# Kernel optimization log

Measured on AMD Instinct MI355X. Metric: run time of the kernel, lower is better.

The kernel has to match this reference:

```python
import math
import jax, jax.numpy as jnp
import numpy as np

B, S, D, H = 4, 1024, 768, 12  # batch, seq, hidden, heads (ViT-Base)
HD = D // H                     # head size = 64
EPS = 1e-12                     # F.normalize eps


def setup_inputs() -> dict:
    key = jax.random.key(0)
    ks = jax.random.split(key, 7)
    s = 0.02
    return {
        "hidden_states": jax.random.normal(ks[0], (B, S, D), dtype=jnp.float32),
        "Wq": jax.random.normal(ks[1], (D, D), dtype=jnp.float32) * s,
        "bq": jax.random.normal(ks[2], (D,), dtype=jnp.float32) * s,
        "Wv": jax.random.normal(ks[3], (D, D), dtype=jnp.float32) * s,
        "bv": jax.random.normal(ks[4], (D,), dtype=jnp.float32) * s,
        "Wo": jax.random.normal(ks[5], (D, D), dtype=jnp.float32) * s,
        "bo": jax.random.normal(ks[6], (D,), dtype=jnp.float32) * s,
    }


def _split_heads(x):
    # [B,S,D] -> [B,H,S,hd]
    b, s, _ = x.shape
    return x.reshape(b, s, H, HD).transpose(0, 2, 1, 3)


def reference(hidden_states, Wq, bq, Wv, bv, Wo, bo):
    b, s, d_model = hidden_states.shape
    # Linear layers (torch Linear: x @ W^T + b; here W stored already transposed)
    mixed_q = hidden_states @ Wq + bq          # key == query in this module
    mixed_v = hidden_states @ Wv + bv
    q = _split_heads(mixed_q)                  # [B,H,S,hd]
    v = _split_heads(mixed_v)                  # [B,H,S,hd]

    # symmetric self-attention (Q @ Q^T)
    scores = jnp.einsum("bhsd,bhtd->bhst", q, q) / math.sqrt(HD)
    probs1 = jax.nn.softmax(scores, axis=-1)                 # [B,H,S,S]
    probs = 0.5 * (probs1 + probs1.transpose(0, 1, 3, 2))    # symmetrize

    # F.normalize(value_layer, dim=2): L2-normalize along the SEQUENCE axis
    vnorm = jnp.maximum(jnp.sqrt(jnp.sum(v * v, axis=2, keepdims=True)), EPS)
    V = v / vnorm                                            # [B,H,S,hd]

    # random-walk Laplacian: D^{-1}(D - P) = I - P / rowsum  (diag structure exploited,
    # same math as diag_embed + matmul in the original)
    dvec = probs.sum(axis=3)                                 # [B,H,S]
    Pn = probs / dvec[..., :, None]                          # D^{-1} P
    LrwV = V - jnp.einsum("bhst,bhtd->bhsd", Pn, V)          # L_rw @ V

    # trace( sum_{b,h} V^T L_rw V ) = sum over all (b,h,s,d) of V * (L_rw V)
    denom = jnp.float32(HD * H * b)
    tr = jnp.abs(jnp.sum(V * LrwV)) / denom

    # orthogonality regularizer: sum (V^T V - I)^2
    VtV = jnp.einsum("bhsd,bhse->bhde", V, V)                # [B,H,hd,hd]
    regular_term = jnp.sum((VtV - jnp.eye(HD, dtype=V.dtype)) ** 2) / denom

    # context = P @ V  (is_last=False)
    ctx = jnp.einsum("bhst,bhtd->bhsd", probs, v)
    ctx = ctx.transpose(0, 2, 1, 3).reshape(b, s, d_model)
    attention_output = ctx @ Wo + bo                         # dropout = identity (p=0)
    return (attention_output, tr, regular_term, mixed_q, mixed_q)
```

## Files before the change

### kernel.cpp

```cpp
#include <hip/hip_runtime.h>
#include <math.h>

constexpr float SCALE = 0.125f;

typedef __attribute__((ext_vector_type(8))) short bf8;
typedef __attribute__((ext_vector_type(8))) unsigned short u16x8;
typedef __attribute__((ext_vector_type(4))) float f32x4;

static __device__ __forceinline__ unsigned short f2bf(float f) {
    unsigned int u = __float_as_uint(f);
    u += 0x7fffu + ((u >> 16) & 1u);
    return (unsigned short)(u >> 16);
}
static __device__ __forceinline__ float bf2f(unsigned short h) {
    return __uint_as_float(((unsigned int)h) << 16);
}
static __device__ __forceinline__ bf8 ld8(const unsigned short* p) {
    return *reinterpret_cast<const bf8*>(p);
}
static __device__ __forceinline__ unsigned int cvtpk(float lo, float hi) {
    unsigned int r;
    asm("v_cvt_pk_bf16_f32 %0, %1, %2" : "=v"(r) : "v"(lo), "v"(hi));
    return r;
}

__global__ __launch_bounds__(256)
void k_prep(const float* __restrict__ Wq, const float* __restrict__ Wv,
            unsigned short* __restrict__ WTq, unsigned short* __restrict__ WTv)
{
    __shared__ unsigned short T[64 * 72];
    const int bid = blockIdx.x;
    const bool isQ = (bid < 144);
    const int lb = isQ ? bid : bid - 144;
    const float* __restrict__ W = isQ ? Wq : Wv;
    unsigned short* __restrict__ WT = isQ ? WTq : WTv;
    const int n0 = (lb % 12) * 64;
    const int k0 = (lb / 12) * 64;
    const int tid = threadIdx.x;
    const int r  = tid >> 2;
    const int c0 = (tid & 3) * 16;
    const float* src = &W[(size_t)(k0 + r) * 768 + n0 + c0];
    #pragma unroll
    for (int q = 0; q < 4; ++q) {
        const float4 v = *reinterpret_cast<const float4*>(src + q * 4);
        uint2 pk;
        pk.x = cvtpk(v.x, v.y);
        pk.y = cvtpk(v.z, v.w);
        *reinterpret_cast<uint2*>(&T[r * 72 + c0 + q * 4]) = pk;
    }
    __syncthreads();
    const int n  = tid >> 2;
    const int kc = (tid & 3) * 16;
    u16x8 o0, o1;
    #pragma unroll
    for (int i = 0; i < 8; ++i) o0[i] = T[(kc + i) * 72 + n];
    #pragma unroll
    for (int i = 0; i < 8; ++i) o1[i] = T[(kc + 8 + i) * 72 + n];
    unsigned short* dst = WT + (size_t)(n0 + n) * 768 + k0 + kc;
    *reinterpret_cast<u16x8*>(dst)     = o0;
    *reinterpret_cast<u16x8*>(dst + 8) = o1;
}

__global__ __launch_bounds__(256)
void k_gemm_qv(const float* __restrict__ X,
               const unsigned short* __restrict__ WTq,
               const unsigned short* __restrict__ WTv,
               const float* __restrict__ bq, const float* __restrict__ bv,
               float* __restrict__ mq1, float* __restrict__ mq2,
               unsigned short* __restrict__ qb, unsigned short* __restrict__ mvb)
{
    __shared__ unsigned short As[64 * 72];
    __shared__ unsigned short Bs[128 * 72];
    const int m0 = blockIdx.x * 64;
    const bool isQ = (blockIdx.y < 6);
    const int n0 = (isQ ? blockIdx.y : blockIdx.y - 6) * 128;
    const unsigned short* __restrict__ WT = isQ ? WTq : WTv;
    const float* __restrict__ bias = isQ ? bq : bv;
    const int tid = threadIdx.x;
    const int wave = tid >> 6, lane = tid & 63, lm = lane & 15, lg = lane >> 4;
    const int wn = wave;

    f32x4 acc[4][2];
    #pragma unroll
    for (int mi = 0; mi < 4; ++mi)
        #pragma unroll
        for (int ni = 0; ni < 2; ++ni) acc[mi][ni] = (f32x4){0.f, 0.f, 0.f, 0.f};

    for (int k0 = 0; k0 < 768; k0 += 64) {
        #pragma unroll
        for (int it = 0; it < 4; ++it) {
            const int idx = tid + it * 256;
            const int arow = idx >> 4;
            const int ac4  = (idx & 15) * 4;
            const float4 v = *reinterpret_cast<const float4*>(
                &X[(size_t)(m0 + arow) * 768 + k0 + ac4]);
            uint2 pk;
            pk.x = cvtpk(v.x, v.y);
            pk.y = cvtpk(v.z, v.w);
            *reinterpret_cast<uint2*>(&As[arow * 72 + ac4]) = pk;
            const int brow = idx >> 3;
            const int bc8  = (idx & 7) * 8;
            *reinterpret_cast<u16x8*>(&Bs[brow * 72 + bc8]) =
                *reinterpret_cast<const u16x8*>(&WT[(size_t)(n0 + brow) * 768 + k0 + bc8]);
        }
        __syncthreads();
        #pragma unroll
        for (int ks = 0; ks < 2; ++ks) {
            bf8 af[4], bfr[2];
            #pragma unroll
            for (int mi = 0; mi < 4; ++mi)
                af[mi] = *reinterpret_cast<const bf8*>(
                    &As[(mi * 16 + lm) * 72 + ks * 32 + lg * 8]);
            #pragma unroll
            for (int ni = 0; ni < 2; ++ni)
                bfr[ni] = *reinterpret_cast<const bf8*>(
                    &Bs[(wn * 32 + ni * 16 + lm) * 72 + ks * 32 + lg * 8]);
            #pragma unroll
            for (int mi = 0; mi < 4; ++mi)
                #pragma unroll
                for (int ni = 0; ni < 2; ++ni)
                    acc[mi][ni] = __builtin_amdgcn_mfma_f32_16x16x32_bf16(
                        af[mi], bfr[ni], acc[mi][ni], 0, 0, 0);
        }
        __syncthreads();
    }
    #pragma unroll
    for (int ni = 0; ni < 2; ++ni) {
        const int c = n0 + wn * 32 + ni * 16 + lm;
        const float bcol = bias[c];
        #pragma unroll
        for (int mi = 0; mi < 4; ++mi)
            #pragma unroll
            for (int j = 0; j < 4; ++j) {
                const int r = m0 + mi * 16 + lg * 4 + j;
                const float v = acc[mi][ni][j] + bcol;
                const size_t off = (size_t)r * 768 + c;
                if (isQ) {
                    mq1[off] = v;
                    mq2[off] = v;
                    qb[off]  = f2bf(v);
                } else {
                    mvb[off] = f2bf(v);
                }
            }
    }
}

__global__ __launch_bounds__(256)
void k_gemm_one(const unsigned short* __restrict__ Xb,
                const unsigned short* __restrict__ WT,
                const float* __restrict__ bias, float* __restrict__ out)
{
    __shared__ unsigned short As[64 * 72];
    __shared__ unsigned short Bs[64 * 72];
    const int m0 = blockIdx.x * 64;
    const int n0 = blockIdx.y * 64;
    const int tid = threadIdx.x;
    const int w = tid >> 6, lane = tid & 63, lm = lane & 15, lg = lane >> 4;

    f32x4 acc[4];
    #pragma unroll
    for (int ni = 0; ni < 4; ++ni) acc[ni] = (f32x4){0.f, 0.f, 0.f, 0.f};

    for (int k0 = 0; k0 < 768; k0 += 64) {
        #pragma unroll
        for (int it = 0; it < 2; ++it) {
            const int idx = tid + it * 256;
            const int row = idx >> 3;
            const int c8  = (idx & 7) * 8;
            *reinterpret_cast<u16x8*>(&As[row * 72 + c8]) =
                *reinterpret_cast<const u16x8*>(&Xb[(size_t)(m0 + row) * 768 + k0 + c8]);
            *reinterpret_cast<u16x8*>(&Bs[row * 72 + c8]) =
                *reinterpret_cast<const u16x8*>(&WT[(size_t)(n0 + row) * 768 + k0 + c8]);
        }
        __syncthreads();
        #pragma unroll
        for (int ks = 0; ks < 2; ++ks) {
            const bf8 af = *reinterpret_cast<const bf8*>(
                &As[(w * 16 + lm) * 72 + ks * 32 + lg * 8]);
            #pragma unroll
            for (int ni = 0; ni < 4; ++ni) {
                const bf8 bfr = *reinterpret_cast<const bf8*>(
                    &Bs[(ni * 16 + lm) * 72 + ks * 32 + lg * 8]);
                acc[ni] = __builtin_amdgcn_mfma_f32_16x16x32_bf16(af, bfr, acc[ni], 0, 0, 0);
            }
        }
        __syncthreads();
    }
    #pragma unroll
    for (int ni = 0; ni < 4; ++ni) {
        const int c = n0 + ni * 16 + lm;
        const float bcol = bias[c];
        #pragma unroll
        for (int j = 0; j < 4; ++j) {
            const int r = m0 + w * 16 + lg * 4 + j;
            out[(size_t)r * 768 + c] = acc[ni][j] + bcol;
        }
    }
}

__global__ __launch_bounds__(256)
void k_pass1T(const unsigned short* __restrict__ qb,
              const unsigned short* __restrict__ mvb,
              unsigned short* __restrict__ vT,
              float* __restrict__ a, float* __restrict__ nrmp)
{
    __shared__ __align__(16) unsigned short Kb[2][64 * 72];
    const int bid = blockIdx.x;
    const int st = (bid >> 3) & 15;
    const int bh = (bid & 7) + 8 * (bid >> 7);
    const int b = bh / 12, h = bh % 12;
    const int s0 = st * 64;
    const int tid = threadIdx.x;
    const int w = tid >> 6, lane = tid & 63, lm = lane & 15, lg = lane >> 4;
    const size_t qoff = (size_t)(b * 1024) * 768 + h * 64;

    {
        const int r  = tid >> 2;
        const int c0 = (tid & 3) * 16;
        const unsigned short* src = mvb + (size_t)(b * 1024 + s0 + r) * 768 + h * 64 + c0;
        const u16x8 x0 = *reinterpret_cast<const u16x8*>(src);
        const u16x8 x1 = *reinterpret_cast<const u16x8*>(src + 8);
        *reinterpret_cast<u16x8*>(&Kb[0][r * 72 + c0])     = x0;
        *reinterpret_cast<u16x8*>(&Kb[0][r * 72 + c0 + 8]) = x1;
        __syncthreads();
        const int dd  = tid >> 2;
        const int sc0 = (tid & 3) * 16;
        u16x8 o0, o1;
        float ps = 0.f;
        #pragma unroll
        for (int k = 0; k < 8; ++k) {
            o0[k] = Kb[0][(sc0 + k) * 72 + dd];
            const float v = bf2f(o0[k]);
            ps = fmaf(v, v, ps);
        }
        #pragma unroll
        for (int k = 0; k < 8; ++k) {
            o1[k] = Kb[0][(sc0 + 8 + k) * 72 + dd];
            const float v = bf2f(o1[k]);
            ps = fmaf(v, v, ps);
        }
        ps += __shfl_xor(ps, 1);
        ps += __shfl_xor(ps, 2);
        if ((tid & 3) == 0) nrmp[(size_t)(bh * 16 + st) * 64 + dd] = ps;
        unsigned short* dst = vT + (size_t)bh * 65536 + (size_t)dd * 1024 + s0 + sc0;
        *reinterpret_cast<u16x8*>(dst)     = o0;
        *reinterpret_cast<u16x8*>(dst + 8) = o1;
        __syncthreads();
    }

    const unsigned short* srow_p = qb + qoff + (size_t)(s0 + 16 * w + lm) * 768;
    const bf8 qs0 = ld8(srow_p + 8 * lg);
    const bf8 qs1 = ld8(srow_p + 32 + 8 * lg);
    const f32x4 z = {0.f, 0.f, 0.f, 0.f};
    float r = 0.f;
    const int sr = tid >> 2;
    const int sc = (tid & 3) << 4;

    u16x8 kr0 = *reinterpret_cast<const u16x8*>(qb + qoff + (size_t)sr * 768 + sc);
    u16x8 kr1 = *reinterpret_cast<const u16x8*>(qb + qoff + (size_t)sr * 768 + sc + 8);
    *reinterpret_cast<u16x8*>(&Kb[0][sr * 72 + sc])     = kr0;
    *reinterpret_cast<u16x8*>(&Kb[0][sr * 72 + sc + 8]) = kr1;
    __syncthreads();
    int cur = 0;

    for (int tt = 0; tt < 16; ++tt) {
        if (tt < 15) {
            const size_t rg = qoff + (size_t)((tt + 1) * 64 + sr) * 768 + sc;
            kr0 = *reinterpret_cast<const u16x8*>(qb + rg);
            kr1 = *reinterpret_cast<const u16x8*>(qb + rg + 8);
        }
        #pragma unroll
        for (int nf = 0; nf < 4; ++nf) {
            const bf8 ka0 = *reinterpret_cast<const bf8*>(
                &Kb[cur][(16 * nf + lm) * 72 + 8 * lg]);
            const bf8 ka1 = *reinterpret_cast<const bf8*>(
                &Kb[cur][(16 * nf + lm) * 72 + 32 + 8 * lg]);
            f32x4 ef = __builtin_amdgcn_mfma_f32_16x16x32_bf16(ka0, qs0, z, 0, 0, 0);
            ef = __builtin_amdgcn_mfma_f32_16x16x32_bf16(ka1, qs1, ef, 0, 0, 0);
            r += __expf(ef[0] * SCALE) + __expf(ef[1] * SCALE)
               + __expf(ef[2] * SCALE) + __expf(ef[3] * SCALE);
        }
        if (tt < 15) {
            *reinterpret_cast<u16x8*>(&Kb[cur ^ 1][sr * 72 + sc])     = kr0;
            *reinterpret_cast<u16x8*>(&Kb[cur ^ 1][sr * 72 + sc + 8]) = kr1;
        }
        __syncthreads();
        cur ^= 1;
    }
    r += __shfl_xor(r, 16);
    r += __shfl_xor(r, 32);
    if (lg == 0) a[(size_t)bh * 1024 + s0 + 16 * w + lm] = 1.f / r;
}

__global__ __launch_bounds__(256)
void k_normfin(const float* __restrict__ nrmp, float* __restrict__ inv_n,
               float* __restrict__ t1p)
{
    const int bh = blockIdx.x;
    const int tid = threadIdx.x;
    __shared__ float t1s[64];
    if (tid < 64) {
        float s = 0.f;
        for (int st = 0; st < 16; ++st)
            s += nrmp[(size_t)(bh * 16 + st) * 64 + tid];
        const float n = fmaxf(sqrtf(s), 1e-12f);
        const float iv = 1.f / n;
        inv_n[bh * 64 + tid] = iv;
        t1s[tid] = s * iv * iv;
    }
    __syncthreads();
    if (tid == 0) {
        float t = 0.f;
        for (int k = 0; k < 64; ++k) t += t1s[k];
        t1p[bh] = t;
    }
}

__global__ __launch_bounds__(256)
void k_pass2(const unsigned short* __restrict__ qb,
             const unsigned short* __restrict__ vT,
             const unsigned short* __restrict__ mvb,
             const float* __restrict__ a,
             const float* __restrict__ invn,
             unsigned short* __restrict__ ctxb,
             float* __restrict__ t2p)
{
    __shared__ __align__(16) unsigned short Kb[2][64 * 72];
    __shared__ __align__(16) unsigned short Vb[2][64 * 72];
    __shared__ __align__(16) unsigned short F_lds[4 * 16 * 72];
    __shared__ float red[256];
    const int bid = blockIdx.x;
    const int st = (bid >> 3) & 15;
    const int bh = (bid & 7) + 8 * (bid >> 7);
    const int b = bh / 12, h = bh % 12;
    const int s0 = st * 64;
    const int tid = threadIdx.x;
    const int w = tid >> 6, lane = tid & 63, lm = lane & 15, lg = lane >> 4;
    const size_t qoff = (size_t)(b * 1024) * 768 + h * 64;
    const unsigned short* srow_p = qb + qoff + (size_t)(s0 + 16 * w + lm) * 768;
    const bf8 qs0 = ld8(srow_p + 8 * lg);
    const bf8 qs1 = ld8(srow_p + 32 + 8 * lg);
    const unsigned short* vbase = vT + (size_t)bh * 65536;
    const float* abase = a + (size_t)bh * 1024;
    const float a_s = abase[s0 + 16 * w + lm];
    unsigned short* Frow = &F_lds[w * 1152 + lm * 72];
    float inv2[4];
    #pragma unroll
    for (int nf = 0; nf < 4; ++nf) {
        const float iv = invn[bh * 64 + lm + 16 * nf];
        inv2[nf] = iv * iv;
    }
    const f32x4 z = {0.f, 0.f, 0.f, 0.f};
    f32x4 acc[4];
    #pragma unroll
    for (int nf = 0; nf < 4; ++nf) acc[nf] = z;
    float sF = 0.f;
    const int sr = tid >> 2;
    const int sc = (tid & 3) << 4;

    u16x8 kr0 = *reinterpret_cast<const u16x8*>(qb + qoff + (size_t)sr * 768 + sc);
    u16x8 kr1 = *reinterpret_cast<const u16x8*>(qb + qoff + (size_t)sr * 768 + sc + 8);
    u16x8 vr0 = *reinterpret_cast<const u16x8*>(vbase + (size_t)sr * 1024 + sc);
    u16x8 vr1 = *reinterpret_cast<const u16x8*>(vbase + (size_t)sr * 1024 + sc + 8);
    *reinterpret_cast<u16x8*>(&Kb[0][sr * 72 + sc])     = kr0;
    *reinterpret_cast<u16x8*>(&Kb[0][sr * 72 + sc + 8]) = kr1;
    *reinterpret_cast<u16x8*>(&Vb[0][sr * 72 + sc])     = vr0;
    *reinterpret_cast<u16x8*>(&Vb[0][sr * 72 + sc + 8]) = vr1;
    __syncthreads();
    int cur = 0;

    for (int tt = 0; tt < 16; ++tt) {
        const int t0 = tt * 64;
        if (tt < 15) {
            const size_t kg = qoff + (size_t)(t0 + 64 + sr) * 768 + sc;
            kr0 = *reinterpret_cast<const u16x8*>(qb + kg);
            kr1 = *reinterpret_cast<const u16x8*>(qb + kg + 8);
            const size_t vg = (size_t)sr * 1024 + t0 + 64 + sc;
            vr0 = *reinterpret_cast<const u16x8*>(vbase + vg);
            vr1 = *reinterpret_cast<const u16x8*>(vbase + vg + 8);
        }
        f32x4 ef[4];
        #pragma unroll
        for (int nf = 0; nf < 4; ++nf) {
            const bf8 ka0 = *reinterpret_cast<const bf8*>(
                &Kb[cur][(16 * nf + lm) * 72 + 8 * lg]);
            const bf8 ka1 = *reinterpret_cast<const bf8*>(
                &Kb[cur][(16 * nf + lm) * 72 + 32 + 8 * lg]);
            ef[nf] = __builtin_amdgcn_mfma_f32_16x16x32_bf16(ka0, qs0, z, 0, 0, 0);
            ef[nf] = __builtin_amdgcn_mfma_f32_16x16x32_bf16(ka1, qs1, ef[nf], 0, 0, 0);
        }
        #pragma unroll
        for (int nf = 0; nf < 4; ++nf) {
            const float4 af = *reinterpret_cast<const float4*>(
                abase + t0 + 16 * nf + 4 * lg);
            const float f0 = __expf(ef[nf][0] * SCALE) * (a_s + af.x);
            const float f1 = __expf(ef[nf][1] * SCALE) * (a_s + af.y);
            const float f2 = __expf(ef[nf][2] * SCALE) * (a_s + af.z);
            const float f3 = __expf(ef[nf][3] * SCALE) * (a_s + af.w);
            sF += (f0 + f1) + (f2 + f3);
            uint2 pk;
            pk.x = cvtpk(f0, f1);
            pk.y = cvtpk(f2, f3);
            *reinterpret_cast<uint2*>(&Frow[16 * nf + 4 * lg]) = pk;
        }
        #pragma unroll
        for (int ks = 0; ks < 2; ++ks) {
            const bf8 fa = *reinterpret_cast<const bf8*>(&Frow[32 * ks + 8 * lg]);
            #pragma unroll
            for (int nf = 0; nf < 4; ++nf) {
                const bf8 vfr = *reinterpret_cast<const bf8*>(
                    &Vb[cur][(16 * nf + lm) * 72 + 32 * ks + 8 * lg]);
                acc[nf] = __builtin_amdgcn_mfma_f32_16x16x32_bf16(fa, vfr, acc[nf], 0, 0, 0);
            }
        }
        if (tt < 15) {
            *reinterpret_cast<u16x8*>(&Kb[cur ^ 1][sr * 72 + sc])     = kr0;
            *reinterpret_cast<u16x8*>(&Kb[cur ^ 1][sr * 72 + sc + 8]) = kr1;
            *reinterpret_cast<u16x8*>(&Vb[cur ^ 1][sr * 72 + sc])     = vr0;
            *reinterpret_cast<u16x8*>(&Vb[cur ^ 1][sr * 72 + sc + 8]) = vr1;
        }
        __syncthreads();
        cur ^= 1;
    }
    sF += __shfl_xor(sF, 16);
    sF += __shfl_xor(sF, 32);

    float t2 = 0.f;
    #pragma unroll
    for (int j = 0; j < 4; ++j) {
        const int srow = s0 + 16 * w + 4 * lg + j;
        const float sFj = __shfl(sF, 4 * lg + j);
        const float rdv = 2.f / sFj;
        const size_t rowoff = (size_t)(b * 1024 + srow) * 768 + h * 64;
        #pragma unroll
        for (int nf = 0; nf < 4; ++nf) {
            const int d = lm + 16 * nf;
            const float cf = 0.5f * acc[nf][j];
            ctxb[rowoff + d] = f2bf(cf);
            const float vv = bf2f(mvb[rowoff + d]);
            t2 = fmaf(vv * cf, inv2[nf] * rdv, t2);
        }
    }
    red[tid] = t2;
    __syncthreads();
    for (int k = 128; k >= 1; k >>= 1) {
        if (tid < k) red[tid] += red[tid + k];
        __syncthreads();
    }
    if (tid == 0) t2p[bh * 16 + st] = red[0];
}

__global__ __launch_bounds__(256)
void k_regwt(const unsigned short* __restrict__ vT, float* __restrict__ Gpart,
             const float* __restrict__ Wo, unsigned short* __restrict__ WTo)
{
    __shared__ unsigned short T[64 * 72];
    const int bid = blockIdx.x;
    const int tid = threadIdx.x;
    if (bid < 384) {
        const int bh = bid >> 3;
        const int q  = bid & 7;
        const int w = tid >> 6, lane = tid & 63, lm = lane & 15, lg = lane >> 4;
        const unsigned short* base = vT + (size_t)bh * 65536;
        const unsigned short* arowp = base + (size_t)(16 * w + lm) * 1024;
        const f32x4 z = {0.f, 0.f, 0.f, 0.f};
        f32x4 acc[4];
        #pragma unroll
        for (int nf = 0; nf < 4; ++nf) acc[nf] = z;
        #pragma unroll
        for (int kk = 0; kk < 4; ++kk) {
            const int t0 = (q * 4 + kk) * 32 + 8 * lg;
            const bf8 av = ld8(arowp + t0);
            #pragma unroll
            for (int nf = 0; nf < 4; ++nf) {
                const bf8 bv = ld8(base + (size_t)(lm + 16 * nf) * 1024 + t0);
                acc[nf] = __builtin_amdgcn_mfma_f32_16x16x32_bf16(av, bv, acc[nf], 0, 0, 0);
            }
        }
        float* gdst = Gpart + (size_t)(bh * 8 + q) * 4096;
        #pragma unroll
        for (int nf = 0; nf < 4; ++nf) {
            const int d2 = lm + 16 * nf;
            #pragma unroll
            for (int j = 0; j < 4; ++j) {
                const int d1 = 16 * w + 4 * lg + j;
                gdst[d1 * 64 + d2] = acc[nf][j];
            }
        }
    } else {
        const int lb = bid - 384;
        const int n0 = (lb % 12) * 64;
        const int k0 = (lb / 12) * 64;
        const int r  = tid >> 2;
        const int c0 = (tid & 3) * 16;
        const float* src = &Wo[(size_t)(k0 + r) * 768 + n0 + c0];
        #pragma unroll
        for (int q = 0; q < 4; ++q) {
            const float4 v = *reinterpret_cast<const float4*>(src + q * 4);
            uint2 pk;
            pk.x = cvtpk(v.x, v.y);
            pk.y = cvtpk(v.z, v.w);
            *reinterpret_cast<uint2*>(&T[r * 72 + c0 + q * 4]) = pk;
        }
        __syncthreads();
        const int n  = tid >> 2;
        const int kc = (tid & 3) * 16;
        u16x8 o0, o1;
        #pragma unroll
        for (int i = 0; i < 8; ++i) o0[i] = T[(kc + i) * 72 + n];
        #pragma unroll
        for (int i = 0; i < 8; ++i) o1[i] = T[(kc + 8 + i) * 72 + n];
        unsigned short* dst = WTo + (size_t)(n0 + n) * 768 + k0 + kc;
        *reinterpret_cast<u16x8*>(dst)     = o0;
        *reinterpret_cast<u16x8*>(dst + 8) = o1;
    }
}

__global__ __launch_bounds__(256)
void k_regfin(const float* __restrict__ Gpart, const float* __restrict__ invn,
              float* __restrict__ regp)
{
    const int bh = blockIdx.x;
    const int tid = threadIdx.x;
    float part = 0.f;
    for (int c = tid; c < 4096; c += 256) {
        const int d1 = c >> 6, d2 = c & 63;
        float g = 0.f;
        #pragma unroll
        for (int q = 0; q < 8; ++q)
            g += Gpart[(size_t)(bh * 8 + q) * 4096 + c];
        g *= invn[bh * 64 + d1] * invn[bh * 64 + d2];
        const float diff = g - ((d1 == d2) ? 1.f : 0.f);
        part = fmaf(diff, diff, part);
    }
    __shared__ float red[256];
    red[tid] = part;
    __syncthreads();
    for (int k = 128; k >= 1; k >>= 1) {
        if (tid < k) red[tid] += red[tid + k];
        __syncthreads();
    }
    if (tid == 0) regp[bh] = red[0];
}

__global__ __launch_bounds__(256)
void k_final(const float* __restrict__ t1p, const float* __restrict__ t2p,
             const float* __restrict__ regp, float* __restrict__ out_tr,
             float* __restrict__ out_reg)
{
    const int tid = threadIdx.x;
    float s1 = 0.f, s2 = 0.f, s3 = 0.f;
    for (int i = tid; i < 768; i += 256) s2 += t2p[i];
    if (tid < 48) { s1 = t1p[tid]; s3 = regp[tid]; }
    __shared__ float R1[256];
    __shared__ float R2[256];
    __shared__ float R3[256];
    R1[tid] = s1; R2[tid] = s2; R3[tid] = s3;
    __syncthreads();
    for (int w = 128; w >= 1; w >>= 1) {
        if (tid < w) { R1[tid] += R1[tid + w]; R2[tid] += R2[tid + w]; R3[tid] += R3[tid + w]; }
        __syncthreads();
    }
    if (tid == 0) {
        *out_tr  = fabsf(R1[0] - R2[0]) / 3072.f;
        *out_reg = R3[0] / 3072.f;
    }
}

extern "C" void kernel_launch(void* const* d_in, const int* in_sizes, int n_in,
                              void* d_out, int out_size, void* d_ws, size_t ws_size,
                              hipStream_t stream)
{
    const float* X  = (const float*)d_in[0];
    const float* Wq = (const float*)d_in[1];
    const float* bq = (const float*)d_in[2];
    const float* Wv = (const float*)d_in[3];
    const float* bv = (const float*)d_in[4];
    const float* Wo = (const float*)d_in[5];
    const float* bo = (const float*)d_in[6];

    float* out = (float*)d_out;
    float* att = out;
    float* tr  = out + 3145728;
    float* rg  = out + 3145729;
    float* mq1 = out + 3145730;
    float* mq2 = out + 6291458;

    float* ws = (float*)d_ws;
    unsigned short* mvb  = (unsigned short*)(ws);
    unsigned short* WTo  = (unsigned short*)(ws);
    unsigned short* qb   = (unsigned short*)(ws + 1572864);
    float*          Gpart = ws + 1572864;
    unsigned short* vTslot = (unsigned short*)(ws + 3145728);
    unsigned short* WTq  = vTslot;
    unsigned short* WTv  = vTslot + 589824;
    unsigned short* vT   = vTslot;
    unsigned short* ctxb = (unsigned short*)(ws + 4718592);
    float* nrmp = ws + 6291456;
    float* aarr = ws + 6389760;
    float* invn = ws + 6438960;
    float* t1p  = ws + 6442032;
    float* t2p  = ws + 6442080;
    float* regp = ws + 6442848;

    if (ws_size < (size_t)6442896 * sizeof(float)) return;

    k_prep     <<<288,          256, 0, stream>>>(Wq, Wv, WTq, WTv);
    k_gemm_qv  <<<dim3(64, 12), 256, 0, stream>>>(X, WTq, WTv, bq, bv, mq1, mq2, qb, mvb);
    k_pass1T   <<<768,          256, 0, stream>>>(qb, mvb, vT, aarr, nrmp);
    k_normfin  <<<48,           256, 0, stream>>>(nrmp, invn, t1p);
    k_pass2    <<<768,          256, 0, stream>>>(qb, vT, mvb, aarr, invn, ctxb, t2p);
    k_regwt    <<<528,          256, 0, stream>>>(vT, Gpart, Wo, WTo);
    k_regfin   <<<48,           256, 0, stream>>>(Gpart, invn, regp);
    k_gemm_one <<<dim3(64, 12), 256, 0, stream>>>(ctxb, WTo, bo, att);
    k_final    <<<1,            256, 0, stream>>>(t1p, t2p, regp, tr, rg);
}
```

Measured before the change: 123.0 us.

## Switch attention passes to 32x32x16 MFMA with register-resident P fragments

Both attention passes now use 32x32x16 bf16 MFMA tiles instead of 16x16x32. Each wave computes a 32x32 block of scores, split across query and key halves. In pass 2 the probability tile is rearranged into A-operand fragments with permlane32_swap, so the LDS staging buffer for F is gone. Partial context results from the two key halves are then summed through LDS and written out as vectorized bf16 rows. This cuts LDS traffic and MFMA instruction count, at the cost of an extra cross-wave reduction, more registers, and reliance on the correct fragment layout.

```diff
diff --git a/kernel.cpp b/kernel.cpp
--- a/kernel.cpp
+++ b/kernel.cpp
@@ -6,6 +6,9 @@
 typedef __attribute__((ext_vector_type(8))) short bf8;
 typedef __attribute__((ext_vector_type(8))) unsigned short u16x8;
 typedef __attribute__((ext_vector_type(4))) float f32x4;
+typedef __attribute__((ext_vector_type(16))) float f32x16;
+typedef __attribute__((ext_vector_type(4))) unsigned int u32x4;
+typedef __attribute__((ext_vector_type(2))) unsigned int u32x2;
 
 static __device__ __forceinline__ unsigned short f2bf(float f) {
     unsigned int u = __float_as_uint(f);
@@ -22,6 +25,11 @@
     unsigned int r;
     asm("v_cvt_pk_bf16_f32 %0, %1, %2" : "=v"(r) : "v"(lo), "v"(hi));
     return r;
+}
+static __device__ __forceinline__ bf8 frag_from(unsigned int d0, unsigned int d1,
+                                                unsigned int d2, unsigned int d3) {
+    u32x4 t; t[0] = d0; t[1] = d1; t[2] = d2; t[3] = d3;
+    return __builtin_bit_cast(bf8, t);
 }
 
 __global__ __launch_bounds__(256)
@@ -206,13 +214,16 @@
               float* __restrict__ a, float* __restrict__ nrmp)
 {
     __shared__ __align__(16) unsigned short Kb[2][64 * 72];
+    __shared__ float rred[4][32];
     const int bid = blockIdx.x;
     const int st = (bid >> 3) & 15;
     const int bh = (bid & 7) + 8 * (bid >> 7);
     const int b = bh / 12, h = bh % 12;
     const int s0 = st * 64;
     const int tid = threadIdx.x;
-    const int w = tid >> 6, lane = tid & 63, lm = lane & 15, lg = lane >> 4;
+    const int w = tid >> 6, lane = tid & 63;
+    const int l31 = lane & 31, hi = lane >> 5;
+    const int sh = w & 1, th = w >> 1;
     const size_t qoff = (size_t)(b * 1024) * 768 + h * 64;
 
     {
@@ -249,48 +260,59 @@
         __syncthreads();
     }
 
-    const unsigned short* srow_p = qb + qoff + (size_t)(s0 + 16 * w + lm) * 768;
-    const bf8 qs0 = ld8(srow_p + 8 * lg);
-    const bf8 qs1 = ld8(srow_p + 32 + 8 * lg);
-    const f32x4 z = {0.f, 0.f, 0.f, 0.f};
-    float r = 0.f;
+    const unsigned short* qrow = qb + qoff + (size_t)(s0 + 32 * sh + l31) * 768;
+    const bf8 qf0 = ld8(qrow + 0  + 8 * hi);
+    const bf8 qf1 = ld8(qrow + 16 + 8 * hi);
+    const bf8 qf2 = ld8(qrow + 32 + 8 * hi);
+    const bf8 qf3 = ld8(qrow + 48 + 8 * hi);
+    f32x16 z16;
+    #pragma unroll
+    for (int i = 0; i < 16; ++i) z16[i] = 0.f;
+    float rs = 0.f;
     const int sr = tid >> 2;
     const int sc = (tid & 3) << 4;
-
-    u16x8 kr0 = *reinterpret_cast<const u16x8*>(qb + qoff + (size_t)sr * 768 + sc);
-    u16x8 kr1 = *reinterpret_cast<const u16x8*>(qb + qoff + (size_t)sr * 768 + sc + 8);
-    *reinterpret_cast<u16x8*>(&Kb[0][sr * 72 + sc])     = kr0;
-    *reinterpret_cast<u16x8*>(&Kb[0][sr * 72 + sc + 8]) = kr1;
+    const int abase_r = (32 * th + l31) * 72 + 8 * hi;
+
+    {
+        const u16x8 k0 = *reinterpret_cast<const u16x8*>(qb + qoff + (size_t)sr * 768 + sc);
+        const u16x8 k1 = *reinterpret_cast<const u16x8*>(qb + qoff + (size_t)sr * 768 + sc + 8);
+        *reinterpret_cast<u16x8*>(&Kb[0][sr * 72 + sc])     = k0;
+        *reinterpret_cast<u16x8*>(&Kb[0][sr * 72 + sc + 8]) = k1;
+    }
     __syncthreads();
     int cur = 0;
 
     for (int tt = 0; tt < 16; ++tt) {
-        if (tt < 15) {
+        u16x8 k0, k1;
+        const bool pf = (tt < 15);
+        if (pf) {
             const size_t rg = qoff + (size_t)((tt + 1) * 64 + sr) * 768 + sc;
-            kr0 = *reinterpret_cast<const u16x8*>(qb + rg);
-            kr1 = *reinterpret_cast<const u16x8*>(qb + rg + 8);
-        }
-        #pragma unroll
-        for (int nf = 0; nf < 4; ++nf) {
-            const bf8 ka0 = *reinterpret_cast<const bf8*>(
-                &Kb[cur][(16 * nf + lm) * 72 + 8 * lg]);
-            const bf8 ka1 = *reinterpret_cast<const bf8*>(
-                &Kb[cur][(16 * nf + lm) * 72 + 32 + 8 * lg]);
-            f32x4 ef = __builtin_amdgcn_mfma_f32_16x16x32_bf16(ka0, qs0, z, 0, 0, 0);
-            ef = __builtin_amdgcn_mfma_f32_16x16x32_bf16(ka1, qs1, ef, 0, 0, 0);
-            r += __expf(ef[0] * SCALE) + __expf(ef[1] * SCALE)
-               + __expf(ef[2] * SCALE) + __expf(ef[3] * SCALE);
-        }
-        if (tt < 15) {
-            *reinterpret_cast<u16x8*>(&Kb[cur ^ 1][sr * 72 + sc])     = kr0;
-            *reinterpret_cast<u16x8*>(&Kb[cur ^ 1][sr * 72 + sc + 8]) = kr1;
+            k0 = *reinterpret_cast<const u16x8*>(qb + rg);
+            k1 = *reinterpret_cast<const u16x8*>(qb + rg + 8);
+        }
+        const bf8 ka0 = *reinterpret_cast<const bf8*>(&Kb[cur][abase_r + 0]);
+        const bf8 ka1 = *reinterpret_cast<const bf8*>(&Kb[cur][abase_r + 16]);
+        const bf8 ka2 = *reinterpret_cast<const bf8*>(&Kb[cur][abase_r + 32]);
+        const bf8 ka3 = *reinterpret_cast<const bf8*>(&Kb[cur][abase_r + 48]);
+        f32x16 ef = __builtin_amdgcn_mfma_f32_32x32x16_bf16(ka0, qf0, z16, 0, 0, 0);
+        ef = __builtin_amdgcn_mfma_f32_32x32x16_bf16(ka1, qf1, ef, 0, 0, 0);
+        ef = __builtin_amdgcn_mfma_f32_32x32x16_bf16(ka2, qf2, ef, 0, 0, 0);
+        ef = __builtin_amdgcn_mfma_f32_32x32x16_bf16(ka3, qf3, ef, 0, 0, 0);
+        #pragma unroll
+        for (int r = 0; r < 16; ++r) rs += __expf(ef[r] * SCALE);
+        if (pf) {
+            *reinterpret_cast<u16x8*>(&Kb[cur ^ 1][sr * 72 + sc])     = k0;
+            *reinterpret_cast<u16x8*>(&Kb[cur ^ 1][sr * 72 + sc + 8]) = k1;
         }
         __syncthreads();
         cur ^= 1;
     }
-    r += __shfl_xor(r, 16);
-    r += __shfl_xor(r, 32);
-    if (lg == 0) a[(size_t)bh * 1024 + s0 + 16 * w + lm] = 1.f / r;
+    rs += __shfl_xor(rs, 32);
+    if (lane < 32) rred[w][l31] = rs;
+    __syncthreads();
+    if (tid < 64)
+        a[(size_t)bh * 1024 + s0 + tid] =
+            1.f / (rred[tid >> 5][tid & 31] + rred[(tid >> 5) + 2][tid & 31]);
 }
 
 __global__ __launch_bounds__(256)
@@ -328,7 +350,7 @@
 {
     __shared__ __align__(16) unsigned short Kb[2][64 * 72];
     __shared__ __align__(16) unsigned short Vb[2][64 * 72];
-    __shared__ __align__(16) unsigned short F_lds[4 * 16 * 72];
+    __shared__ float sFred[4][32];
     __shared__ float red[256];
     const int bid = blockIdx.x;
     const int st = (bid >> 3) & 15;
@@ -336,112 +358,163 @@
     const int b = bh / 12, h = bh % 12;
     const int s0 = st * 64;
     const int tid = threadIdx.x;
-    const int w = tid >> 6, lane = tid & 63, lm = lane & 15, lg = lane >> 4;
+    const int w = tid >> 6, lane = tid & 63;
+    const int l31 = lane & 31, hi = lane >> 5;
+    const int sh = w & 1, th = w >> 1;
     const size_t qoff = (size_t)(b * 1024) * 768 + h * 64;
-    const unsigned short* srow_p = qb + qoff + (size_t)(s0 + 16 * w + lm) * 768;
-    const bf8 qs0 = ld8(srow_p + 8 * lg);
-    const bf8 qs1 = ld8(srow_p + 32 + 8 * lg);
     const unsigned short* vbase = vT + (size_t)bh * 65536;
     const float* abase = a + (size_t)bh * 1024;
-    const float a_s = abase[s0 + 16 * w + lm];
-    unsigned short* Frow = &F_lds[w * 1152 + lm * 72];
-    float inv2[4];
-    #pragma unroll
-    for (int nf = 0; nf < 4; ++nf) {
-        const float iv = invn[bh * 64 + lm + 16 * nf];
-        inv2[nf] = iv * iv;
-    }
-    const f32x4 z = {0.f, 0.f, 0.f, 0.f};
-    f32x4 acc[4];
-    #pragma unroll
-    for (int nf = 0; nf < 4; ++nf) acc[nf] = z;
-    float sF = 0.f;
+
+    const unsigned short* qrow = qb + qoff + (size_t)(s0 + 32 * sh + l31) * 768;
+    const bf8 qf0 = ld8(qrow + 0  + 8 * hi);
+    const bf8 qf1 = ld8(qrow + 16 + 8 * hi);
+    const bf8 qf2 = ld8(qrow + 32 + 8 * hi);
+    const bf8 qf3 = ld8(qrow + 48 + 8 * hi);
+    const float a_s = abase[s0 + 32 * sh + l31];
+    f32x16 z16;
+    #pragma unroll
+    for (int i = 0; i < 16; ++i) z16[i] = 0.f;
+    f32x16 paccA = z16, paccB = z16;
+    float sFl = 0.f;
     const int sr = tid >> 2;
     const int sc = (tid & 3) << 4;
-
-    u16x8 kr0 = *reinterpret_cast<const u16x8*>(qb + qoff + (size_t)sr * 768 + sc);
-    u16x8 kr1 = *reinterpret_cast<const u16x8*>(qb + qoff + (size_t)sr * 768 + sc + 8);
-    u16x8 vr0 = *reinterpret_cast<const u16x8*>(vbase + (size_t)sr * 1024 + sc);
-    u16x8 vr1 = *reinterpret_cast<const u16x8*>(vbase + (size_t)sr * 1024 + sc + 8);
-    *reinterpret_cast<u16x8*>(&Kb[0][sr * 72 + sc])     = kr0;
-    *reinterpret_cast<u16x8*>(&Kb[0][sr * 72 + sc + 8]) = kr1;
-    *reinterpret_cast<u16x8*>(&Vb[0][sr * 72 + sc])     = vr0;
-    *reinterpret_cast<u16x8*>(&Vb[0][sr * 72 + sc + 8]) = vr1;
+    const int krow = (32 * th + l31) * 72 + 8 * hi;
+    const int vrow0 = l31 * 72 + 32 * th + 8 * hi;
+    const int vrow1 = (32 + l31) * 72 + 32 * th + 8 * hi;
+
+    {
+        const u16x8 k0 = *reinterpret_cast<const u16x8*>(qb + qoff + (size_t)sr * 768 + sc);
+        const u16x8 k1 = *reinterpret_cast<const u16x8*>(qb + qoff + (size_t)sr * 768 + sc + 8);
+        const u16x8 v0 = *reinterpret_cast<const u16x8*>(vbase + (size_t)sr * 1024 + sc);
+        const u16x8 v1 = *reinterpret_cast<const u16x8*>(vbase + (size_t)sr * 1024 + sc + 8);
+        *reinterpret_cast<u16x8*>(&Kb[0][sr * 72 + sc])     = k0;
+        *reinterpret_cast<u16x8*>(&Kb[0][sr * 72 + sc + 8]) = k1;
+        *reinterpret_cast<u16x8*>(&Vb[0][sr * 72 + sc])     = v0;
+        *reinterpret_cast<u16x8*>(&Vb[0][sr * 72 + sc + 8]) = v1;
+    }
     __syncthreads();
     int cur = 0;
 
     for (int tt = 0; tt < 16; ++tt) {
         const int t0 = tt * 64;
-        if (tt < 15) {
+        u16x8 k0, k1, v0, v1;
+        const bool pf = (tt < 15);
+        if (pf) {
             const size_t kg = qoff + (size_t)(t0 + 64 + sr) * 768 + sc;
-            kr0 = *reinterpret_cast<const u16x8*>(qb + kg);
-            kr1 = *reinterpret_cast<const u16x8*>(qb + kg + 8);
+            k0 = *reinterpret_cast<const u16x8*>(qb + kg);
+            k1 = *reinterpret_cast<const u16x8*>(qb + kg + 8);
             const size_t vg = (size_t)sr * 1024 + t0 + 64 + sc;
-            vr0 = *reinterpret_cast<const u16x8*>(vbase + vg);
-            vr1 = *reinterpret_cast<const u16x8*>(vbase + vg + 8);
-        }
-        f32x4 ef[4];
-        #pragma unroll
-        for (int nf = 0; nf < 4; ++nf) {
-            const bf8 ka0 = *reinterpret_cast<const bf8*>(
-                &Kb[cur][(16 * nf + lm) * 72 + 8 * lg]);
-            const bf8 ka1 = *reinterpret_cast<const bf8*>(
-                &Kb[cur][(16 * nf + lm) * 72 + 32 + 8 * lg]);
-            ef[nf] = __builtin_amdgcn_mfma_f32_16x16x32_bf16(ka0, qs0, z, 0, 0, 0);
-            ef[nf] = __builtin_amdgcn_mfma_f32_16x16x32_bf16(ka1, qs1, ef[nf], 0, 0, 0);
-        }
-        #pragma unroll
-        for (int nf = 0; nf < 4; ++nf) {
-            const float4 af = *reinterpret_cast<const float4*>(
-                abase + t0 + 16 * nf + 4 * lg);
-            const float f0 = __expf(ef[nf][0] * SCALE) * (a_s + af.x);
-            const float f1 = __expf(ef[nf][1] * SCALE) * (a_s + af.y);
-            const float f2 = __expf(ef[nf][2] * SCALE) * (a_s + af.z);
-            const float f3 = __expf(ef[nf][3] * SCALE) * (a_s + af.w);
-            sF += (f0 + f1) + (f2 + f3);
-            uint2 pk;
-            pk.x = cvtpk(f0, f1);
-            pk.y = cvtpk(f2, f3);
-            *reinterpret_cast<uint2*>(&Frow[16 * nf + 4 * lg]) = pk;
-        }
-        #pragma unroll
-        for (int ks = 0; ks < 2; ++ks) {
-            const bf8 fa = *reinterpret_cast<const bf8*>(&Frow[32 * ks + 8 * lg]);
-            #pragma unroll
-            for (int nf = 0; nf < 4; ++nf) {
-                const bf8 vfr = *reinterpret_cast<const bf8*>(
-                    &Vb[cur][(16 * nf + lm) * 72 + 32 * ks + 8 * lg]);
-                acc[nf] = __builtin_amdgcn_mfma_f32_16x16x32_bf16(fa, vfr, acc[nf], 0, 0, 0);
-            }
-        }
-        if (tt < 15) {
-            *reinterpret_cast<u16x8*>(&Kb[cur ^ 1][sr * 72 + sc])     = kr0;
-            *reinterpret_cast<u16x8*>(&Kb[cur ^ 1][sr * 72 + sc + 8]) = kr1;
-            *reinterpret_cast<u16x8*>(&Vb[cur ^ 1][sr * 72 + sc])     = vr0;
-            *reinterpret_cast<u16x8*>(&Vb[cur ^ 1][sr * 72 + sc + 8]) = vr1;
+            v0 = *reinterpret_cast<const u16x8*>(vbase + vg);
+            v1 = *reinterpret_cast<const u16x8*>(vbase + vg + 8);
+        }
+        const bf8 ka0 = *reinterpret_cast<const bf8*>(&Kb[cur][krow + 0]);
+        const bf8 ka1 = *reinterpret_cast<const bf8*>(&Kb[cur][krow + 16]);
+        const bf8 ka2 = *reinterpret_cast<const bf8*>(&Kb[cur][krow + 32]);
+        const bf8 ka3 = *reinterpret_cast<const bf8*>(&Kb[cur][krow + 48]);
+        f32x16 ef = __builtin_amdgcn_mfma_f32_32x32x16_bf16(ka0, qf0, z16, 0, 0, 0);
+        ef = __builtin_amdgcn_mfma_f32_32x32x16_bf16(ka1, qf1, ef, 0, 0, 0);
+        ef = __builtin_amdgcn_mfma_f32_32x32x16_bf16(ka2, qf2, ef, 0, 0, 0);
+        ef = __builtin_amdgcn_mfma_f32_32x32x16_bf16(ka3, qf3, ef, 0, 0, 0);
+        const float* ab = abase + t0 + 32 * th + 4 * hi;
+        unsigned int pk[8];
+        {
+            const float4 a40 = *reinterpret_cast<const float4*>(ab);
+            const float4 a41 = *reinterpret_cast<const float4*>(ab + 8);
+            const float4 a42 = *reinterpret_cast<const float4*>(ab + 16);
+            const float4 a43 = *reinterpret_cast<const float4*>(ab + 24);
+            float f0, f1, f2, f3;
+            #define FGRP(g, a4)                                               \
+                f0 = __expf(ef[4*g+0] * SCALE) * (a_s + a4.x);                \
+                f1 = __expf(ef[4*g+1] * SCALE) * (a_s + a4.y);                \
+                f2 = __expf(ef[4*g+2] * SCALE) * (a_s + a4.z);                \
+                f3 = __expf(ef[4*g+3] * SCALE) * (a_s + a4.w);                \
+                sFl += (f0 + f1) + (f2 + f3);                                 \
+                pk[2*g]     = cvtpk(f0, f1);                                  \
+                pk[2*g + 1] = cvtpk(f2, f3);
+            FGRP(0, a40)
+            FGRP(1, a41)
+            FGRP(2, a42)
+            FGRP(3, a43)
+            #undef FGRP
+        }
+        const u32x2 s1 = __builtin_amdgcn_permlane32_swap(pk[0], pk[2], false, false);
+        const u32x2 s2 = __builtin_amdgcn_permlane32_swap(pk[1], pk[3], false, false);
+        const u32x2 s3 = __builtin_amdgcn_permlane32_swap(pk[4], pk[6], false, false);
+        const u32x2 s4 = __builtin_amdgcn_permlane32_swap(pk[5], pk[7], false, false);
+        const bf8 fa0 = frag_from(s1[0], s2[0], s1[1], s2[1]);
+        const bf8 fa1 = frag_from(s3[0], s4[0], s3[1], s4[1]);
+        {
+            const bf8 bv00 = *reinterpret_cast<const bf8*>(&Vb[cur][vrow0]);
+            const bf8 bv01 = *reinterpret_cast<const bf8*>(&Vb[cur][vrow0 + 16]);
+            const bf8 bv10 = *reinterpret_cast<const bf8*>(&Vb[cur][vrow1]);
+            const bf8 bv11 = *reinterpret_cast<const bf8*>(&Vb[cur][vrow1 + 16]);
+            paccA = __builtin_amdgcn_mfma_f32_32x32x16_bf16(fa0, bv00, paccA, 0, 0, 0);
+            paccA = __builtin_amdgcn_mfma_f32_32x32x16_bf16(fa1, bv01, paccA, 0, 0, 0);
+            paccB = __builtin_amdgcn_mfma_f32_32x32x16_bf16(fa0, bv10, paccB, 0, 0, 0);
+            paccB = __builtin_amdgcn_mfma_f32_32x32x16_bf16(fa1, bv11, paccB, 0, 0, 0);
+        }
+        if (pf) {
+            *reinterpret_cast<u16x8*>(&Kb[cur ^ 1][sr * 72 + sc])     = k0;
+            *reinterpret_cast<u16x8*>(&Kb[cur ^ 1][sr * 72 + sc + 8]) = k1;
+            *reinterpret_cast<u16x8*>(&Vb[cur ^ 1][sr * 72 + sc])     = v0;
+            *reinterpret_cast<u16x8*>(&Vb[cur ^ 1][sr * 72 + sc + 8]) = v1;
         }
         __syncthreads();
         cur ^= 1;
     }
-    sF += __shfl_xor(sF, 16);
-    sF += __shfl_xor(sF, 32);
-
+
+    sFl += __shfl_xor(sFl, 32);
+    if (lane < 32) sFred[w][l31] = sFl;
+
+    float* ctxA = reinterpret_cast<float*>(&Kb[0][0]);
+    float* ctxB = ctxA + 32 * 66;
+    float* dst = (sh == 0) ? ctxA : ctxB;
+    if (th == 0) {
+        #pragma unroll
+        for (int r = 0; r < 16; ++r) {
+            const int i = (r & 3) + 8 * (r >> 2) + 4 * hi;
+            dst[i * 66 + l31]      = paccA[r];
+            dst[i * 66 + 32 + l31] = paccB[r];
+        }
+    }
+    __syncthreads();
+    if (th == 1) {
+        #pragma unroll
+        for (int r = 0; r < 16; ++r) {
+            const int i = (r & 3) + 8 * (r >> 2) + 4 * hi;
+            dst[i * 66 + l31]      += paccA[r];
+            dst[i * 66 + 32 + l31] += paccB[r];
+        }
+    }
+    __syncthreads();
+
+    const int es  = tid >> 2;
+    const int ed0 = (tid & 3) * 16;
+    const int le  = es & 31;
+    const float sFt = sFred[es >> 5][le] + sFred[(es >> 5) + 2][le];
+    const float rdv = 2.f / sFt;
+    const float* ctxP = (es < 32) ? ctxA : ctxB;
+    const size_t rowoff = (size_t)(b * 1024 + s0 + es) * 768 + h * 64 + ed0;
+    const u16x8 mv0 = *reinterpret_cast<const u16x8*>(mvb + rowoff);
+    const u16x8 mv1 = *reinterpret_cast<const u16x8*>(mvb + rowoff + 8);
     float t2 = 0.f;
-    #pragma unroll
-    for (int j = 0; j < 4; ++j) {
-        const int srow = s0 + 16 * w + 4 * lg + j;
-        const float sFj = __shfl(sF, 4 * lg + j);
-        const float rdv = 2.f / sFj;
-        const size_t rowoff = (size_t)(b * 1024 + srow) * 768 + h * 64;
-        #pragma unroll
-        for (int nf = 0; nf < 4; ++nf) {
-            const int d = lm + 16 * nf;
-            const float cf = 0.5f * acc[nf][j];
-            ctxb[rowoff + d] = f2bf(cf);
-            const float vv = bf2f(mvb[rowoff + d]);
-            t2 = fmaf(vv * cf, inv2[nf] * rdv, t2);
-        }
-    }
+    u16x8 o0, o1;
+    #pragma unroll
+    for (int jj = 0; jj < 8; ++jj) {
+        const float cv = 0.5f * ctxP[le * 66 + ed0 + jj];
+        o0[jj] = f2bf(cv);
+        const float iv = invn[bh * 64 + ed0 + jj];
+        t2 = fmaf(bf2f(mv0[jj]) * cv, iv * iv * rdv, t2);
+    }
+    #pragma unroll
+    for (int jj = 0; jj < 8; ++jj) {
+        const float cv = 0.5f * ctxP[le * 66 + ed0 + 8 + jj];
+        o1[jj] = f2bf(cv);
+        const float iv = invn[bh * 64 + ed0 + 8 + jj];
+        t2 = fmaf(bf2f(mv1[jj]) * cv, iv * iv * rdv, t2);
+    }
+    *reinterpret_cast<u16x8*>(ctxb + rowoff)     = o0;
+    *reinterpret_cast<u16x8*>(ctxb + rowoff + 8) = o1;
     red[tid] = t2;
     __syncthreads();
     for (int k = 128; k >= 1; k >>= 1) {
```

Measured after the change: 125.0 us. Within noise of the previous version (+1.6%).
